# Optimization experiments

Hardware: AMD Instinct MI355X
Metric: run time of the kernel (lower is better)

## Reference

```python
import jax, jax.numpy as jnp
import numpy as np

RADIUS = 0.1
K = 32  # num_neighbors


def setup_inputs() -> dict:
    key = jax.random.key(0)
    k1, k2, k3 = jax.random.split(key, 3)
    B, N, M, C = 4, 16384, 4096, 64
    points_coords = jax.random.uniform(k1, (B, 3, N), dtype=jnp.float32)
    centers_coords = jax.random.uniform(k2, (B, 3, M), dtype=jnp.float32)
    points_features = jax.random.normal(k3, (B, C, N), dtype=jnp.float32)
    return {
        "points_coords": points_coords,
        "centers_coords": centers_coords,
        "points_features": points_features,
    }


def _ball_query_indices(points_coords, centers_coords, radius, k):
    """Return [B, M, K] int32 indices of up to k points within radius of each
    center; slots beyond the in-ball count are padded with the first in-ball
    index (0 if the ball is empty), matching PVCNN's ball_query semantics."""
    B, _, N = points_coords.shape
    # squared pairwise distances [B, M, N]
    p2 = jnp.sum(points_coords * points_coords, axis=1)          # [B, N]
    c2 = jnp.sum(centers_coords * centers_coords, axis=1)        # [B, M]
    cp = jnp.einsum('bdm,bdn->bmn', centers_coords, points_coords)
    d2 = c2[:, :, None] + p2[None if False else slice(None), None, :] - 2.0 * cp
    valid = d2 < (radius * radius)
    # candidate index if in ball, else sentinel N; first k in index order
    cand = jnp.where(valid, jnp.arange(N, dtype=jnp.int32)[None, None, :],
                     jnp.int32(N))
    topk = -jax.lax.top_k(-cand, k)[0]                           # ascending
    first = topk[..., :1]
    idx = jnp.where(topk == N, first, topk)   # pad with first in-ball index
    idx = jnp.where(idx == N, 0, idx)         # empty ball -> index 0
    return idx


def _group(feat, idx):
    # feat: [B, C, N], idx: [B, M, K] -> [B, C, M, K]
    return jax.vmap(lambda f, i: f[:, i])(feat, idx)


def reference(points_coords, centers_coords, points_features):
    idx = _ball_query_indices(points_coords, centers_coords, RADIUS, K)
    idx = jax.lax.stop_gradient(idx)
    # relative neighbor coordinates [B, 3, M, K]
    neighbor_coords = _group(points_coords, idx) - centers_coords[:, :, :, None]
    neighbor_features = _group(points_features, idx)             # [B, C, M, K]
    return jnp.concatenate([neighbor_coords, neighbor_features], axis=1)
```

## Files before the change

### kernel.cpp

```cpp
#include <hip/hip_runtime.h>
#include <climits>

#define KNN 32
#define NPTS 16384
#define MCTR 4096
#define BATCH 4
#define CFEAT 64
#define NBINS 1000
#define HITCAP 128
#define CPW 4
#define WCHUNKS 8
#define FPAD 34

typedef float f4 __attribute__((ext_vector_type(4)));

__device__ __forceinline__ bool ball_pred(float cx, float cy, float cz, float c2,
                                          float px, float py, float pz) {
    const float r2 = 0.009999999776482582f;
    const float p2 = __fmaf_rn(pz, pz, __fmaf_rn(px, px, __fmul_rn(py, py)));
    const float cp = __fmaf_rn(cz, pz, __fmaf_rn(cy, py, __fmul_rn(cx, px)));
    const float d2 = __fsub_rn(__fadd_rn(c2, p2), __fmul_rn(2.0f, cp));
    return d2 < r2;
}

__device__ __forceinline__ int bin_of(float x, float y, float z) {
    int bx = min(max((int)(x * 10.0f), 0), 9);
    int by = min(max((int)(y * 10.0f), 0), 9);
    int bz = min(max((int)(z * 10.0f), 0), 9);
    return (bx * 10 + by) * 10 + bz;
}

__global__ __launch_bounds__(1024) void bin_prep(
    const float* __restrict__ points,
    int* __restrict__ binStart,
    f4* __restrict__ sP,
    f4* __restrict__ pointsT)
{
    __shared__ int hist[NBINS];
    __shared__ int scanbuf[1024];
    const int b = blockIdx.x;
    const int t = threadIdx.x;
    const float* pc = points + (size_t)b * 3 * NPTS;
    const size_t gb = (size_t)b * NPTS;

    if (t < NBINS) hist[t] = 0;
    __syncthreads();

    f4 myp[16];
    int mybin[16];
#pragma unroll
    for (int r = 0; r < 16; ++r) {
        const int i = r * 1024 + t;
        const float x = pc[i], y = pc[NPTS + i], z = pc[2 * NPTS + i];
        myp[r] = (f4){x, y, z, __int_as_float(i)};
        pointsT[gb + i] = (f4){x, y, z, 0.0f};
        const int bn = bin_of(x, y, z);
        mybin[r] = bn;
        atomicAdd(&hist[bn], 1);
    }
    __syncthreads();

    const int v = (t < NBINS) ? hist[t] : 0;
    scanbuf[t] = v;
    __syncthreads();
    for (int off = 1; off < 1024; off <<= 1) {
        const int u = (t >= off) ? scanbuf[t - off] : 0;
        __syncthreads();
        scanbuf[t] += u;
        __syncthreads();
    }
    const int excl = scanbuf[t] - v;
    if (t < NBINS) {
        binStart[b * (NBINS + 1) + t] = excl;
    }
    if (t == 0) binStart[b * (NBINS + 1) + NBINS] = NPTS;
    __syncthreads();
    if (t < NBINS) hist[t] = excl;
    __syncthreads();

#pragma unroll
    for (int r = 0; r < 16; ++r) {
        const int pos = atomicAdd(&hist[mybin[r]], 1);
        sP[gb + pos] = myp[r];
    }
}

__global__ __launch_bounds__(256) void transpose_kernel(
    const float* __restrict__ feats, float* __restrict__ featsT)
{
    __shared__ float tl[64][65];
    const int b  = blockIdx.x >> 8;
    const int n0 = (blockIdx.x & 255) * 64;
    const float* f = feats  + (size_t)b * CFEAT * NPTS;
    float* ft      = featsT + (size_t)b * NPTS * CFEAT;
    const int t = threadIdx.x;
    const int nl = t & 63, cq = t >> 6;
#pragma unroll
    for (int r = 0; r < 16; ++r) {
        const int ch = r * 4 + cq;
        tl[ch][nl] = __builtin_nontemporal_load(&f[(size_t)ch * NPTS + n0 + nl]);
    }
    __syncthreads();
    const int quad = t & 15;
    const int ngrp = t >> 4;
#pragma unroll
    for (int r = 0; r < 4; ++r) {
        const int n = r * 16 + ngrp;
        f4 o;
        o.x = tl[4 * quad + 0][n];
        o.y = tl[4 * quad + 1][n];
        o.z = tl[4 * quad + 2][n];
        o.w = tl[4 * quad + 3][n];
        *reinterpret_cast<f4*>(&ft[(size_t)(n0 + n) * CFEAT + 4 * quad]) = o;
    }
}

__global__ __launch_bounds__(64) void bq_gather_fused(
    const float* __restrict__ points, const float* __restrict__ centers,
    const int* __restrict__ binStart, const f4* __restrict__ sP,
    const f4* __restrict__ pointsT, const float* __restrict__ featsT,
    float* __restrict__ out)
{
    __shared__ int hits[HITCAP];
    __shared__ float lfeat[KNN][FPAD];
    const int lane = threadIdx.x;
    const int cls = blockIdx.x & 7;
    const int b   = cls >> 1;
    const int m   = ((cls & 1) << 11) | (blockIdx.x >> 3);

    const float* cc = centers + (size_t)b * 3 * MCTR;
    const float cx = cc[m], cy = cc[MCTR + m], cz = cc[2 * MCTR + m];
    const float c2 = __fmaf_rn(cz, cz, __fmaf_rn(cx, cx, __fmul_rn(cy, cy)));

    hits[lane] = INT_MAX;
    hits[lane + 64] = INT_MAX;

    const float rg = 0.1001f;
    const int xlo = max((int)((cx - rg) * 10.0f), 0), xhi = min((int)((cx + rg) * 10.0f), 9);
    const int ylo = max((int)((cy - rg) * 10.0f), 0), yhi = min((int)((cy + rg) * 10.0f), 9);
    const int zlo = max((int)((cz - rg) * 10.0f), 0), zhi = min((int)((cz + rg) * 10.0f), 9);

    const int base = b * NPTS;
    const int* bs = binStart + b * (NBINS + 1);
    int cnt = 0;

    for (int X = xlo; X <= xhi; ++X) {
        for (int Y = ylo; Y <= yhi; ++Y) {
            const int cb = (X * 10 + Y) * 10;
            const int s = bs[cb + zlo];
            const int e = bs[cb + zhi + 1];
            for (int p = s; p < e; p += 64) {
                const int o = p + lane;
                const bool in = o < e;
                const f4 P = in ? sP[base + o] : (f4){1e9f, 1e9f, 1e9f, 0.0f};
                const bool valid = in && ball_pred(cx, cy, cz, c2, P.x, P.y, P.z);
                const unsigned long long mask = __ballot(valid);
                if (mask) {
                    const int prefix = __popcll(mask & ((1ull << lane) - 1ull));
                    const int ppos = cnt + prefix;
                    if (valid && ppos < HITCAP) hits[ppos] = __float_as_int(P.w);
                    cnt += __popcll(mask);
                }
            }
        }
    }

    int fidx;
    if (cnt > HITCAP) {
        const float* pc = points + (size_t)b * 3 * NPTS;
        int cnt2 = 0, firstIdx = 0;
        for (int j0 = 0; j0 < NPTS; j0 += 64) {
            const int j = j0 + lane;
            const bool valid = ball_pred(cx, cy, cz, c2, pc[j], pc[NPTS + j], pc[2 * NPTS + j]);
            const unsigned long long mask = __ballot(valid);
            if (mask) {
                if (cnt2 == 0) firstIdx = j0 + __builtin_ctzll(mask);
                const int prefix = __popcll(mask & ((1ull << lane) - 1ull));
                if (valid && (cnt2 + prefix) < KNN) hits[cnt2 + prefix] = j;
                cnt2 += __popcll(mask);
                if (cnt2 >= KNN) break;
            }
        }
        const int first = (cnt2 == 0) ? 0 : firstIdx;
        fidx = (lane < cnt2 && lane < KNN) ? hits[lane] : first;
    } else {
        int a  = hits[lane];
        int v2 = hits[lane + 64];
#pragma unroll
        for (int k = 2; k <= 128; k <<= 1) {
#pragma unroll
            for (int j = 64; j >= 1; j >>= 1) {
                if (j > (k >> 1)) continue;
                if (j == 64) {
                    const int lo = min(a, v2), hi = max(a, v2);
                    a = lo; v2 = hi;
                } else {
                    const bool lower = (lane & j) == 0;
                    const bool upA = (lane & k) == 0;
                    const bool upB = ((lane + 64) & k) == 0;
                    const int va = __shfl_xor(a, j);
                    a = (lower == upA) ? min(a, va) : max(a, va);
                    const int vb = __shfl_xor(v2, j);
                    v2 = (lower == upB) ? min(v2, vb) : max(v2, vb);
                }
            }
        }
        const int first = __shfl(a, 0);
        fidx = (lane < cnt) ? a : ((cnt == 0) ? 0 : first);
    }

    float* obase = out + ((size_t)b * 67 * MCTR + m) * KNN;

    if (lane < 32) {
        const f4 P = pointsT[(size_t)base + fidx];
        obase[lane]                          = P.x - cx;
        obase[(size_t)MCTR * KNN + lane]     = P.y - cy;
        obase[(size_t)2 * MCTR * KNN + lane] = P.z - cz;
    }

    const float* ft = featsT + (size_t)b * NPTS * CFEAT;
    const int pp = lane >> 3;
    const int q  = lane & 7;
    const int ch8 = lane >> 3;
    const int kq  = lane & 7;
#pragma unroll
    for (int h = 0; h < 2; ++h) {
#pragma unroll
        for (int s = 0; s < 4; ++s) {
            const int k = s * 8 + pp;
            const int ik = __shfl(fidx, k);
            const float4 v = *reinterpret_cast<const float4*>(
                ft + (size_t)ik * CFEAT + h * 32 + q * 4);
            *reinterpret_cast<float2*>(&lfeat[k][4 * q])     = make_float2(v.x, v.y);
            *reinterpret_cast<float2*>(&lfeat[k][4 * q + 2]) = make_float2(v.z, v.w);
        }
#pragma unroll
        for (int it = 0; it < 4; ++it) {
            const int cw = it * 8 + ch8;
            const int ch = h * 32 + cw;
            float4 o;
            o.x = lfeat[4 * kq + 0][cw];
            o.y = lfeat[4 * kq + 1][cw];
            o.z = lfeat[4 * kq + 2][cw];
            o.w = lfeat[4 * kq + 3][cw];
            *reinterpret_cast<float4*>(&obase[(size_t)(3 + ch) * MCTR * KNN + 4 * kq]) = o;
        }
    }
}

__global__ __launch_bounds__(256) void ball_query_kernel(
    const float* __restrict__ points, const float* __restrict__ centers,
    int* __restrict__ idx_out)
{
    const int wave = (blockIdx.x * blockDim.x + threadIdx.x) >> 6;
    const int lane = threadIdx.x & 63;
    const int wavesPerBatch = MCTR / CPW;
    const int b = wave / wavesPerBatch;
    const int m0 = (wave % wavesPerBatch) * CPW;

    const float* pc = points + (size_t)b * 3 * NPTS;
    const float* cc = centers + (size_t)b * 3 * MCTR;

    float cx[CPW], cy[CPW], cz[CPW], c2[CPW];
    int cnt[CPW], firstIdx[CPW];
#pragma unroll
    for (int c = 0; c < CPW; ++c) {
        cx[c] = cc[m0 + c]; cy[c] = cc[MCTR + m0 + c]; cz[c] = cc[2 * MCTR + m0 + c];
        c2[c] = __fmaf_rn(cz[c], cz[c], __fmaf_rn(cx[c], cx[c], __fmul_rn(cy[c], cy[c])));
        cnt[c] = 0; firstIdx[c] = 0;
    }
    int* outbase = idx_out + ((size_t)b * MCTR + m0) * KNN;

    for (int w = 0; w < NPTS / (64 * WCHUNKS); ++w) {
        const int base = w * 64 * WCHUNKS + lane;
        float px[WCHUNKS], py[WCHUNKS], pz[WCHUNKS];
#pragma unroll
        for (int u = 0; u < WCHUNKS; ++u) {
            px[u] = pc[base + 64 * u];
            py[u] = pc[NPTS + base + 64 * u];
            pz[u] = pc[2 * NPTS + base + 64 * u];
        }
#pragma unroll
        for (int u = 0; u < WCHUNKS; ++u) {
            const int j0 = w * 64 * WCHUNKS + 64 * u;
            const int j = j0 + lane;
#pragma unroll
            for (int c = 0; c < CPW; ++c) {
                const bool valid = ball_pred(cx[c], cy[c], cz[c], c2[c], px[u], py[u], pz[u]);
                const unsigned long long mask = __ballot(valid);
                if (mask) {
                    if (cnt[c] == 0) firstIdx[c] = j0 + __builtin_ctzll(mask);
                    const int prefix = __popcll(mask & ((1ull << lane) - 1ull));
                    if (valid && (cnt[c] + prefix) < KNN)
                        outbase[c * KNN + cnt[c] + prefix] = j;
                    cnt[c] += __popcll(mask);
                }
            }
        }
        bool alldone = true;
#pragma unroll
        for (int c = 0; c < CPW; ++c) alldone &= (cnt[c] >= KNN);
        if (alldone) break;
    }
#pragma unroll
    for (int c = 0; c < CPW; ++c) {
        if (cnt[c] < KNN && lane >= cnt[c] && lane < KNN)
            outbase[c * KNN + lane] = firstIdx[c];
    }
}

__global__ __launch_bounds__(256) void gather_direct_kernel(
    const float* __restrict__ points, const float* __restrict__ centers,
    const float* __restrict__ feats, const int* __restrict__ idx,
    float* __restrict__ out)
{
    const long long t = (long long)blockIdx.x * blockDim.x + threadIdx.x;
    const int k = (int)(t & (KNN - 1));
    long long r = t >> 5;
    const int m = (int)(r & (MCTR - 1));
    r >>= 12;
    const int ch = (int)(r % 67);
    const int b = (int)(r / 67);
    const int i = idx[((size_t)(b * MCTR + m)) * KNN + k];
    float v;
    if (ch < 3) {
        v = points[(size_t)b * 3 * NPTS + (size_t)ch * NPTS + i]
          - centers[(size_t)b * 3 * MCTR + (size_t)ch * MCTR + m];
    } else {
        v = feats[(size_t)b * CFEAT * NPTS + (size_t)(ch - 3) * NPTS + i];
    }
    out[t] = v;
}

extern "C" void kernel_launch(void* const* d_in, const int* in_sizes, int n_in,
                              void* d_out, int out_size, void* d_ws, size_t ws_size,
                              hipStream_t stream) {
    const float* points  = nullptr;
    const float* centers = nullptr;
    const float* feats   = nullptr;
    for (int i = 0; i < n_in; ++i) {
        if (in_sizes[i] == BATCH * 3 * NPTS)      points  = (const float*)d_in[i];
        else if (in_sizes[i] == BATCH * 3 * MCTR) centers = (const float*)d_in[i];
        else if (in_sizes[i] == BATCH * CFEAT * NPTS) feats = (const float*)d_in[i];
    }
    float* out = (float*)d_out;

    size_t off = 0;
    auto carve = [&](size_t bytes) -> void* {
        void* p = (char*)d_ws + off;
        off = (off + bytes + 255) & ~(size_t)255;
        return p;
    };
    int*   idx      = (int*)  carve((size_t)BATCH * MCTR * KNN * 4);
    float* featsT   = (float*)carve((size_t)BATCH * NPTS * CFEAT * 4);
    int*   binStart = (int*)  carve((size_t)BATCH * (NBINS + 1) * 4);
    f4*    sP       = (f4*)   carve((size_t)BATCH * NPTS * 16);
    f4*    pointsT  = (f4*)   carve((size_t)BATCH * NPTS * 16);
    const size_t neededFull = off;

    if (ws_size >= neededFull) {
        bin_prep<<<BATCH, 1024, 0, stream>>>(points, binStart, sP, pointsT);
        transpose_kernel<<<BATCH * (NPTS / 64), 256, 0, stream>>>(feats, featsT);
        bq_gather_fused<<<BATCH * MCTR, 64, 0, stream>>>(
            points, centers, binStart, sP, pointsT, featsT, out);
    } else {
        const int nThreads1 = (BATCH * MCTR / CPW) * 64;
        ball_query_kernel<<<nThreads1 / 256, 256, 0, stream>>>(points, centers, idx);
        const long long total = (long long)BATCH * 67 * MCTR * KNN;
        gather_direct_kernel<<<(int)(total / 256), 256, 0, stream>>>(points, centers, feats, idx, out);
    }
}
```

Before: 70.30 us.

## Merge bin prep and feature transpose into one launch; use nontemporal output stores

```diff
diff --git a/kernel.cpp b/kernel.cpp
--- a/kernel.cpp
+++ b/kernel.cpp
@@ -30,16 +30,44 @@
     return (bx * 10 + by) * 10 + bz;
 }
 
-__global__ __launch_bounds__(1024) void bin_prep(
-    const float* __restrict__ points,
-    int* __restrict__ binStart,
-    f4* __restrict__ sP,
-    f4* __restrict__ pointsT)
+__global__ __launch_bounds__(1024) void prep_all(
+    const float* __restrict__ feats, float* __restrict__ featsT,
+    const float* __restrict__ points, int* __restrict__ binStart,
+    f4* __restrict__ sP, f4* __restrict__ pointsT)
 {
+    __shared__ float tl[64][65];
     __shared__ int hist[NBINS];
     __shared__ int scanbuf[1024];
-    const int b = blockIdx.x;
+
     const int t = threadIdx.x;
+    if (blockIdx.x < BATCH * 64) {
+        const int blk = blockIdx.x;
+        const int b = blk >> 6;
+        const int n_base = (blk & 63) * 256;
+        const float* f = feats  + (size_t)b * CFEAT * NPTS;
+        float* ft      = featsT + (size_t)b * NPTS * CFEAT;
+        const int nl = t & 63, cq = t >> 6;
+        const int quad = t & 15, n_s = t >> 4;
+        for (int tile = 0; tile < 4; ++tile) {
+            const int n0 = n_base + tile * 64;
+#pragma unroll
+            for (int r = 0; r < 4; ++r) {
+                const int ch = r * 16 + cq;
+                tl[ch][nl] = __builtin_nontemporal_load(&f[(size_t)ch * NPTS + n0 + nl]);
+            }
+            __syncthreads();
+            f4 o;
+            o.x = tl[4 * quad + 0][n_s];
+            o.y = tl[4 * quad + 1][n_s];
+            o.z = tl[4 * quad + 2][n_s];
+            o.w = tl[4 * quad + 3][n_s];
+            *reinterpret_cast<f4*>(&ft[(size_t)(n0 + n_s) * CFEAT + 4 * quad]) = o;
+            __syncthreads();
+        }
+        return;
+    }
+
+    const int b = blockIdx.x - BATCH * 64;
     const float* pc = points + (size_t)b * 3 * NPTS;
     const size_t gb = (size_t)b * NPTS;
 
@@ -70,10 +98,8 @@
         __syncthreads();
     }
     const int excl = scanbuf[t] - v;
-    if (t < NBINS) {
-        binStart[b * (NBINS + 1) + t] = excl;
-    }
-    if (t == 0) binStart[b * (NBINS + 1) + NBINS] = NPTS;
+    if (t < NBINS) binStart[b * (NBINS + 1) + t] = excl;
+    if (t == 0)    binStart[b * (NBINS + 1) + NBINS] = NPTS;
     __syncthreads();
     if (t < NBINS) hist[t] = excl;
     __syncthreads();
@@ -82,36 +108,6 @@
     for (int r = 0; r < 16; ++r) {
         const int pos = atomicAdd(&hist[mybin[r]], 1);
         sP[gb + pos] = myp[r];
-    }
-}
-
-__global__ __launch_bounds__(256) void transpose_kernel(
-    const float* __restrict__ feats, float* __restrict__ featsT)
-{
-    __shared__ float tl[64][65];
-    const int b  = blockIdx.x >> 8;
-    const int n0 = (blockIdx.x & 255) * 64;
-    const float* f = feats  + (size_t)b * CFEAT * NPTS;
-    float* ft      = featsT + (size_t)b * NPTS * CFEAT;
-    const int t = threadIdx.x;
-    const int nl = t & 63, cq = t >> 6;
-#pragma unroll
-    for (int r = 0; r < 16; ++r) {
-        const int ch = r * 4 + cq;
-        tl[ch][nl] = __builtin_nontemporal_load(&f[(size_t)ch * NPTS + n0 + nl]);
-    }
-    __syncthreads();
-    const int quad = t & 15;
-    const int ngrp = t >> 4;
-#pragma unroll
-    for (int r = 0; r < 4; ++r) {
-        const int n = r * 16 + ngrp;
-        f4 o;
-        o.x = tl[4 * quad + 0][n];
-        o.y = tl[4 * quad + 1][n];
-        o.z = tl[4 * quad + 2][n];
-        o.w = tl[4 * quad + 3][n];
-        *reinterpret_cast<f4*>(&ft[(size_t)(n0 + n) * CFEAT + 4 * quad]) = o;
     }
 }
 
@@ -213,9 +209,9 @@
 
     if (lane < 32) {
         const f4 P = pointsT[(size_t)base + fidx];
-        obase[lane]                          = P.x - cx;
-        obase[(size_t)MCTR * KNN + lane]     = P.y - cy;
-        obase[(size_t)2 * MCTR * KNN + lane] = P.z - cz;
+        __builtin_nontemporal_store(P.x - cx, &obase[lane]);
+        __builtin_nontemporal_store(P.y - cy, &obase[(size_t)MCTR * KNN + lane]);
+        __builtin_nontemporal_store(P.z - cz, &obase[(size_t)2 * MCTR * KNN + lane]);
     }
 
     const float* ft = featsT + (size_t)b * NPTS * CFEAT;
@@ -238,12 +234,13 @@
         for (int it = 0; it < 4; ++it) {
             const int cw = it * 8 + ch8;
             const int ch = h * 32 + cw;
-            float4 o;
+            f4 o;
             o.x = lfeat[4 * kq + 0][cw];
             o.y = lfeat[4 * kq + 1][cw];
             o.z = lfeat[4 * kq + 2][cw];
             o.w = lfeat[4 * kq + 3][cw];
-            *reinterpret_cast<float4*>(&obase[(size_t)(3 + ch) * MCTR * KNN + 4 * kq]) = o;
+            __builtin_nontemporal_store(o,
+                reinterpret_cast<f4*>(&obase[(size_t)(3 + ch) * MCTR * KNN + 4 * kq]));
         }
     }
 }
@@ -359,8 +356,8 @@
     const size_t neededFull = off;
 
     if (ws_size >= neededFull) {
-        bin_prep<<<BATCH, 1024, 0, stream>>>(points, binStart, sP, pointsT);
-        transpose_kernel<<<BATCH * (NPTS / 64), 256, 0, stream>>>(feats, featsT);
+        prep_all<<<BATCH * 64 + BATCH, 1024, 0, stream>>>(
+            feats, featsT, points, binStart, sP, pointsT);
         bq_gather_fused<<<BATCH * MCTR, 64, 0, stream>>>(
             points, centers, binStart, sP, pointsT, featsT, out);
     } else {
```

New measurement: 61.98 us. -11.8%, faster.
